# Optimization experiments

Hardware: AMD Instinct MI355X
Metric: run time of the kernel (lower is better)

Reference implementation:

```python
import jax, jax.numpy as jnp
import numpy as np

EMB = 512
HEAD = 8
HEAD_DIM = EMB // HEAD


def setup_inputs() -> dict:
    key = jax.random.key(0)
    ks = jax.random.split(key, 12)
    B, S = 2, 4096
    scale = 1.0 / np.sqrt(EMB)
    inp = {
        "q": jax.random.normal(ks[0], (B, S, EMB), dtype=jnp.float32),
        "kv": jax.random.normal(ks[1], (B, S, EMB), dtype=jnp.float32),
        "Wq": jax.random.normal(ks[2], (EMB, EMB), dtype=jnp.float32) * scale,
        "bq": jax.random.normal(ks[3], (EMB,), dtype=jnp.float32) * 0.01,
        "Wk": jax.random.normal(ks[4], (EMB, EMB), dtype=jnp.float32) * scale,
        "bk": jax.random.normal(ks[5], (EMB,), dtype=jnp.float32) * 0.01,
        "Wv": jax.random.normal(ks[6], (EMB, EMB), dtype=jnp.float32) * scale,
        "bv": jax.random.normal(ks[7], (EMB,), dtype=jnp.float32) * 0.01,
        "Wo": jax.random.normal(ks[8], (EMB, EMB), dtype=jnp.float32) * scale,
        "bo": jax.random.normal(ks[9], (EMB,), dtype=jnp.float32) * 0.01,
    }
    return inp


def reference(q, kv, Wq, bq, Wk, bk, Wv, bv, Wo, bo):
    B, N, _ = q.shape
    M = kv.shape[1]
    # Linear projections (torch Linear: x @ W^T + b)
    qh = (q @ Wq.T + bq).reshape(B, N, HEAD, HEAD_DIM).transpose(0, 2, 1, 3)  # [B,H,N,d]
    kh = (kv @ Wk.T + bk).reshape(B, M, HEAD, HEAD_DIM).transpose(0, 2, 1, 3)  # [B,H,M,d]
    vh = (kv @ Wv.T + bv).reshape(B, M, HEAD, HEAD_DIM).transpose(0, 2, 1, 3)  # [B,H,M,d]
    attn = jnp.einsum("bhnd,bhmd->bhnm", qh, kh) / jnp.sqrt(jnp.float32(HEAD_DIM))
    attn = jax.nn.softmax(attn, axis=-1)
    out = jnp.einsum("bhnm,bhmd->bhnd", attn, vh)  # [B,H,N,d]
    out = out.transpose(0, 2, 1, 3).reshape(B, N, EMB)
    out = out @ Wo.T + bo
    return out
```

## Files before the change

kernel.cpp:

```cpp
#include <hip/hip_runtime.h>
#include <stdint.h>

typedef unsigned short u16;
typedef __attribute__((ext_vector_type(8))) short short8;
typedef __attribute__((ext_vector_type(4))) float f32x4;
typedef __attribute__((ext_vector_type(16))) float f32x16;

typedef __attribute__((address_space(1))) void as1_void;
typedef __attribute__((address_space(3))) void as3_void;

__device__ inline u16 f2bf(float x) {
  uint32_t u = __float_as_uint(x);
  return (u16)((u + 0x7fffu + ((u >> 16) & 1u)) >> 16);
}

__device__ inline void gload16(const void* g, void* l) {
  __builtin_amdgcn_global_load_lds((as1_void*)g, (as3_void*)l, 16, 0, 0);
}

__device__ inline uint32_t cvtpk(float lo, float hi) {
  uint32_t d;
  asm("v_cvt_pk_bf16_f32 %0, %1, %2" : "=v"(d) : "v"(lo), "v"(hi));
  return d;
}

__device__ inline void plswap(uint32_t& a, uint32_t& b) {
  asm("v_permlane32_swap_b32 %0, %1" : "+v"(a), "+v"(b));
}

__device__ inline float fexp2(float x) {
  float r;
  asm("v_exp_f32 %0, %1" : "=v"(r) : "v"(x));
  return r;
}

__global__ __launch_bounds__(256) void cvt_all(const float* __restrict__ q,
                                               const float* __restrict__ kv,
                                               const float* __restrict__ Wq,
                                               const float* __restrict__ Wk,
                                               const float* __restrict__ Wv,
                                               const float* __restrict__ Wo,
                                               u16* __restrict__ qb,
                                               u16* __restrict__ kvb,
                                               u16* __restrict__ wall) {
  const int bx = blockIdx.x;
  const float* in;
  u16* out;
  int i;
  if (bx < 4096) {
    in = q; out = qb; i = bx * 256 + threadIdx.x;
  } else if (bx < 8192) {
    in = kv; out = kvb; i = (bx - 4096) * 256 + threadIdx.x;
  } else {
    int widx = (bx - 8192) >> 8;
    in = (widx == 0) ? Wq : (widx == 1) ? Wk : (widx == 2) ? Wv : Wo;
    out = wall + (size_t)widx * 262144;
    i = ((bx - 8192) & 255) * 256 + threadIdx.x;
  }
  float4 v = ((const float4*)in)[i];
  ushort4 o;
  o.x = f2bf(v.x); o.y = f2bf(v.y); o.z = f2bf(v.z); o.w = f2bf(v.w);
  ((ushort4*)out)[i] = o;
}

__global__ __launch_bounds__(256) void gemm_qkv(const u16* __restrict__ qb,
                                                const u16* __restrict__ kvb,
                                                const u16* __restrict__ wq,
                                                const u16* __restrict__ wk,
                                                const u16* __restrict__ wv,
                                                const float* __restrict__ bq,
                                                const float* __restrict__ bk,
                                                const float* __restrict__ bv,
                                                u16* __restrict__ Qh,
                                                u16* __restrict__ Kh,
                                                u16* __restrict__ Vt, float qscale) {
  __shared__ u16 Al[128 * 32];
  __shared__ u16 Wl[128 * 32];
  const int z = blockIdx.z;
  const u16* A = (z == 0) ? qb : kvb;
  const u16* W = (z == 0) ? wq : (z == 1) ? wk : wv;
  const float* bias = (z == 0) ? bq : (z == 1) ? bk : bv;
  const float prescale = (z == 0) ? qscale : 1.0f;
  u16* Cout = (z == 0) ? Qh : (z == 1) ? Kh : Vt;

  const int tid = threadIdx.x;
  const int lane = tid & 63;
  const int wv_ = tid >> 6;
  const int c = lane & 15;
  const int g = lane >> 4;
  const int wr = wv_ >> 1, wc = wv_ & 1;
  const int m0 = blockIdx.x * 128;
  const int n0 = blockIdx.y * 128;

  f32x4 acc[4][4];
#pragma unroll
  for (int i = 0; i < 4; i++)
#pragma unroll
    for (int j = 0; j < 4; j++) acc[i][j] = (f32x4){0.f, 0.f, 0.f, 0.f};

  for (int kk = 0; kk < 512; kk += 32) {
    __syncthreads();
    {
      int t0 = tid;
      int r0 = t0 >> 2, c0 = t0 & 3;
      gload16(A + (size_t)(m0 + r0) * 512 + kk + c0 * 8, (char*)Al + (size_t)(wv_ * 64) * 16);
      gload16(W + (size_t)(n0 + r0) * 512 + kk + c0 * 8, (char*)Wl + (size_t)(wv_ * 64) * 16);
      int t1 = 256 + tid;
      int r1 = t1 >> 2, c1 = t1 & 3;
      gload16(A + (size_t)(m0 + r1) * 512 + kk + c1 * 8, (char*)Al + (size_t)(256 + wv_ * 64) * 16);
      gload16(W + (size_t)(n0 + r1) * 512 + kk + c1 * 8, (char*)Wl + (size_t)(256 + wv_ * 64) * 16);
    }
    __syncthreads();

    short8 af[4], wf[4];
#pragma unroll
    for (int ai = 0; ai < 4; ai++)
      af[ai] = *(const short8*)&Al[(wr * 64 + ai * 16 + c) * 32 + g * 8];
#pragma unroll
    for (int bj = 0; bj < 4; bj++)
      wf[bj] = *(const short8*)&Wl[(wc * 64 + bj * 16 + c) * 32 + g * 8];
#pragma unroll
    for (int ai = 0; ai < 4; ai++)
#pragma unroll
      for (int bj = 0; bj < 4; bj++)
        acc[ai][bj] = __builtin_amdgcn_mfma_f32_16x16x32_bf16(af[ai], wf[bj], acc[ai][bj], 0, 0, 0);
  }

#pragma unroll
  for (int ai = 0; ai < 4; ai++)
#pragma unroll
    for (int bj = 0; bj < 4; bj++)
#pragma unroll
      for (int r = 0; r < 4; r++) {
        int m = m0 + wr * 64 + ai * 16 + g * 4 + r;
        int n = n0 + wc * 64 + bj * 16 + c;
        float v = (acc[ai][bj][r] + bias[n]) * prescale;
        int b = m >> 12, s = m & 4095;
        int h = n >> 6, d = n & 63;
        size_t idx;
        if (z < 2)
          idx = ((size_t)(b * 8 + h) * 4096 + s) * 64 + d;
        else
          idx = ((size_t)(b * 8 + h) * 64 + d) * 4096 + s;
        Cout[idx] = f2bf(v);
      }
}

__global__ __launch_bounds__(256) void gemm_out(const u16* __restrict__ A,
                                                const u16* __restrict__ W,
                                                const float* __restrict__ bias,
                                                float* __restrict__ Cout) {
  __shared__ u16 Al[128 * 32];
  __shared__ u16 Wl[128 * 32];
  const int tid = threadIdx.x;
  const int lane = tid & 63;
  const int wv_ = tid >> 6;
  const int c = lane & 15;
  const int g = lane >> 4;
  const int wr = wv_ >> 1, wc = wv_ & 1;
  const int m0 = blockIdx.x * 128;
  const int n0 = blockIdx.y * 128;

  f32x4 acc[4][4];
#pragma unroll
  for (int i = 0; i < 4; i++)
#pragma unroll
    for (int j = 0; j < 4; j++) acc[i][j] = (f32x4){0.f, 0.f, 0.f, 0.f};

  for (int kk = 0; kk < 512; kk += 32) {
    __syncthreads();
    {
      int t0 = tid;
      int r0 = t0 >> 2, c0 = t0 & 3;
      gload16(A + (size_t)(m0 + r0) * 512 + kk + c0 * 8, (char*)Al + (size_t)(wv_ * 64) * 16);
      gload16(W + (size_t)(n0 + r0) * 512 + kk + c0 * 8, (char*)Wl + (size_t)(wv_ * 64) * 16);
      int t1 = 256 + tid;
      int r1 = t1 >> 2, c1 = t1 & 3;
      gload16(A + (size_t)(m0 + r1) * 512 + kk + c1 * 8, (char*)Al + (size_t)(256 + wv_ * 64) * 16);
      gload16(W + (size_t)(n0 + r1) * 512 + kk + c1 * 8, (char*)Wl + (size_t)(256 + wv_ * 64) * 16);
    }
    __syncthreads();

    short8 af[4], wf[4];
#pragma unroll
    for (int ai = 0; ai < 4; ai++)
      af[ai] = *(const short8*)&Al[(wr * 64 + ai * 16 + c) * 32 + g * 8];
#pragma unroll
    for (int bj = 0; bj < 4; bj++)
      wf[bj] = *(const short8*)&Wl[(wc * 64 + bj * 16 + c) * 32 + g * 8];
#pragma unroll
    for (int ai = 0; ai < 4; ai++)
#pragma unroll
      for (int bj = 0; bj < 4; bj++)
        acc[ai][bj] = __builtin_amdgcn_mfma_f32_16x16x32_bf16(af[ai], wf[bj], acc[ai][bj], 0, 0, 0);
  }

#pragma unroll
  for (int ai = 0; ai < 4; ai++)
#pragma unroll
    for (int bj = 0; bj < 4; bj++)
#pragma unroll
      for (int r = 0; r < 4; r++) {
        int m = m0 + wr * 64 + ai * 16 + g * 4 + r;
        int n = n0 + wc * 64 + bj * 16 + c;
        Cout[(size_t)m * 512 + n] = acc[ai][bj][r] + bias[n];
      }
}

__global__ __launch_bounds__(256) void attn_split(const u16* __restrict__ Qh,
                                                  const u16* __restrict__ Kh,
                                                  const u16* __restrict__ Vt,
                                                  float* __restrict__ Op,
                                                  float* __restrict__ Ml) {
  __shared__ __align__(16) char smem[32768];
  const int tid = threadIdx.x;
  const int lane = tid & 63;
  const int w = tid >> 6;
  const int c5 = lane & 31;
  const int h = lane >> 5;
  const int bid = (blockIdx.x & 7) * 128 + (blockIdx.x >> 3);
  const int half = bid & 1;
  const int qt = (bid >> 1) & 31;
  const int bh = bid >> 6;
  const int q0 = qt * 128 + w * 32;
  const u16* Qb = Qh + (size_t)bh * 262144;
  const u16* Kb = Kh + (size_t)bh * 262144 + (size_t)half * 2048 * 64;
  const u16* Vb = Vt + (size_t)bh * 262144 + half * 2048;

  short8 qf[4];
#pragma unroll
  for (int kd = 0; kd < 4; kd++)
    qf[kd] = *(const short8*)(Qb + (size_t)(q0 + c5) * 64 + kd * 16 + h * 8);

  f32x16 accO[2];
#pragma unroll
  for (int i = 0; i < 16; i++) { accO[0][i] = 0.f; accO[1][i] = 0.f; }
  float l_r = 0.f;

  const int r = tid >> 4, p = tid & 15;
  const int x = p ^ r;
  const int gb = x >> 3, ge = x & 7;
  const u16* srcKA = Kb + (size_t)(r + 32 * gb) * 64 + ge * 8;
  const u16* srcKB = Kb + (size_t)(16 + r + 32 * gb) * 64 + ge * 8;
  const u16* srcVA = Vb + (size_t)(r + 32 * gb) * 4096 + ge * 8;
  const u16* srcVB = Vb + (size_t)(16 + r + 32 * gb) * 4096 + ge * 8;

#define ATTN_STAGE(BUF, T)                                \
  {                                                       \
    char* b_ = (char*)smem + (BUF)*16384 + w * 1024;      \
    gload16(srcKA + (size_t)(T)*4096, b_);                \
    gload16(srcKB + (size_t)(T)*4096, b_ + 4096);         \
    gload16(srcVA + (T)*64, b_ + 8192);                   \
    gload16(srcVB + (T)*64, b_ + 12288);                  \
  }

  ATTN_STAGE(0, 0)
  __syncthreads();
  int cur = 0;
  const int swz = c5 & 15;
  const int rowb = c5 * 128;

  for (int t = 0; t < 32; ++t) {
    if (t < 31) ATTN_STAGE(cur ^ 1, t + 1)

    const u16* Kl = (const u16*)(smem + cur * 16384);
    const u16* Vl = Kl + 4096;

    f32x16 s0, s1;
#pragma unroll
    for (int i = 0; i < 16; i++) { s0[i] = 0.f; s1[i] = 0.f; }
    __builtin_amdgcn_s_setprio(1);
#pragma unroll
    for (int kd = 0; kd < 4; kd++) {
      short8 kf0 = *(const short8*)&Kl[rowb + ((((kd << 1) + h) ^ swz) << 3)];
      short8 kf1 = *(const short8*)&Kl[rowb + (((8 + (kd << 1) + h) ^ swz) << 3)];
      s0 = __builtin_amdgcn_mfma_f32_32x32x16_bf16(kf0, qf[kd], s0, 0, 0, 0);
      s1 = __builtin_amdgcn_mfma_f32_32x32x16_bf16(kf1, qf[kd], s1, 0, 0, 0);
    }
    __builtin_amdgcn_s_setprio(0);

#pragma unroll
    for (int i = 0; i < 16; i++) { s0[i] = fexp2(s0[i]); s1[i] = fexp2(s1[i]); }

    float tsum0 = ((s0[0] + s1[0]) + (s0[4] + s1[4])) + ((s0[8] + s1[8]) + (s0[12] + s1[12]));
    float tsum1 = ((s0[1] + s1[1]) + (s0[5] + s1[5])) + ((s0[9] + s1[9]) + (s0[13] + s1[13]));
    float tsum2 = ((s0[2] + s1[2]) + (s0[6] + s1[6])) + ((s0[10] + s1[10]) + (s0[14] + s1[14]));
    float tsum3 = ((s0[3] + s1[3]) + (s0[7] + s1[7])) + ((s0[11] + s1[11]) + (s0[15] + s1[15]));
    float rsq = (tsum0 + tsum1) + (tsum2 + tsum3);
    l_r += rsq + __shfl_xor(rsq, 32);

    uint32_t pk0[4][2], pk1[4][2];
#pragma unroll
    for (int u = 0; u < 4; u++) {
      pk0[u][0] = cvtpk(s0[4 * u], s0[4 * u + 1]);
      pk0[u][1] = cvtpk(s0[4 * u + 2], s0[4 * u + 3]);
      pk1[u][0] = cvtpk(s1[4 * u], s1[4 * u + 1]);
      pk1[u][1] = cvtpk(s1[4 * u + 2], s1[4 * u + 3]);
    }
    short8 pa[4];
#pragma unroll
    for (int km = 0; km < 2; km++) {
      const int uA = (km & 1) * 2, uB = uA + 1;
      uint32_t a0 = pk0[uA][0], b0 = pk0[uB][0]; plswap(a0, b0);
      uint32_t a1 = pk0[uA][1], b1 = pk0[uB][1]; plswap(a1, b1);
      union { uint32_t u[4]; short8 s; } uu;
      uu.u[0] = a0; uu.u[1] = a1; uu.u[2] = b0; uu.u[3] = b1;
      pa[km] = uu.s;
    }
#pragma unroll
    for (int km = 2; km < 4; km++) {
      const int uA = (km & 1) * 2, uB = uA + 1;
      uint32_t a0 = pk1[uA][0], b0 = pk1[uB][0]; plswap(a0, b0);
      uint32_t a1 = pk1[uA][1], b1 = pk1[uB][1]; plswap(a1, b1);
      union { uint32_t u[4]; short8 s; } uu;
      uu.u[0] = a0; uu.u[1] = a1; uu.u[2] = b0; uu.u[3] = b1;
      pa[km] = uu.s;
    }

    __builtin_amdgcn_s_setprio(1);
#pragma unroll
    for (int km = 0; km < 4; km++) {
      short8 vf0 = *(const short8*)&Vl[rowb + ((((km << 1) + h) ^ swz) << 3)];
      short8 vf1 = *(const short8*)&Vl[rowb + (((8 + (km << 1) + h) ^ swz) << 3)];
      accO[0] = __builtin_amdgcn_mfma_f32_32x32x16_bf16(vf0, pa[km], accO[0], 0, 0, 0);
      accO[1] = __builtin_amdgcn_mfma_f32_32x32x16_bf16(vf1, pa[km], accO[1], 0, 0, 0);
    }
    __builtin_amdgcn_s_setprio(0);

    __syncthreads();
    cur ^= 1;
  }

  const size_t pbase = (size_t)(half * 16 + bh) * 4096 + q0 + c5;
  float* Opw = Op + pbase * 64;
#pragma unroll
  for (int db = 0; db < 2; db++)
#pragma unroll
    for (int rr = 0; rr < 16; rr++) {
      int d = db * 32 + 4 * h + (rr & 3) + 8 * (rr >> 2);
      Opw[d] = accO[db][rr];
    }
  if (h == 0) { Ml[pbase * 2] = 0.f; Ml[pbase * 2 + 1] = l_r; }
}

__global__ __launch_bounds__(256) void attn_combine(const float* __restrict__ Op,
                                                    const float* __restrict__ Ml,
                                                    u16* __restrict__ aO) {
  int tg = blockIdx.x * 256 + threadIdx.x;
  int bhq = tg >> 3, seg = tg & 7;
  const float* p0 = Op + (size_t)bhq * 64 + seg * 8;
  const float* p1 = p0 + 4194304;
  float m0 = Ml[bhq * 2], l0 = Ml[bhq * 2 + 1];
  float m1 = Ml[131072 + bhq * 2], l1 = Ml[131072 + bhq * 2 + 1];
  float ms = fmaxf(m0, m1);
  float a0 = fexp2(m0 - ms), a1 = fexp2(m1 - ms);
  float inv = 1.f / (l0 * a0 + l1 * a1);
  float4 x0 = ((const float4*)p0)[0], x1 = ((const float4*)p0)[1];
  float4 y0 = ((const float4*)p1)[0], y1 = ((const float4*)p1)[1];
  ushort4 o0, o1;
  o0.x = f2bf((x0.x * a0 + y0.x * a1) * inv);
  o0.y = f2bf((x0.y * a0 + y0.y * a1) * inv);
  o0.z = f2bf((x0.z * a0 + y0.z * a1) * inv);
  o0.w = f2bf((x0.w * a0 + y0.w * a1) * inv);
  o1.x = f2bf((x1.x * a0 + y1.x * a1) * inv);
  o1.y = f2bf((x1.y * a0 + y1.y * a1) * inv);
  o1.z = f2bf((x1.z * a0 + y1.z * a1) * inv);
  o1.w = f2bf((x1.w * a0 + y1.w * a1) * inv);
  int bh = bhq >> 12, q = bhq & 4095;
  int b = bh >> 3, hh = bh & 7;
  u16* dst = aO + ((size_t)(b * 4096 + q)) * 512 + hh * 64 + seg * 8;
  ((ushort4*)dst)[0] = o0;
  ((ushort4*)dst)[1] = o1;
}

extern "C" void kernel_launch(void* const* d_in, const int* in_sizes, int n_in,
                              void* d_out, int out_size, void* d_ws, size_t ws_size,
                              hipStream_t stream) {
  const float* q  = (const float*)d_in[0];
  const float* kv = (const float*)d_in[1];
  const float* Wq = (const float*)d_in[2];
  const float* bq = (const float*)d_in[3];
  const float* Wk = (const float*)d_in[4];
  const float* bk = (const float*)d_in[5];
  const float* Wv = (const float*)d_in[6];
  const float* bv = (const float*)d_in[7];
  const float* Wo = (const float*)d_in[8];
  const float* bo = (const float*)d_in[9];

  const size_t MB = 1u << 20;
  char* ws = (char*)d_ws;
  u16* qb  = (u16*)(ws + 0 * MB);
  u16* kvb = (u16*)(ws + 8 * MB);
  u16* wqb = (u16*)(ws + 16 * MB);
  u16* wkb = (u16*)(ws + 16 * MB + 524288);
  u16* wvb = (u16*)(ws + 17 * MB);
  u16* wob = (u16*)(ws + 17 * MB + 524288);
  u16* Qh  = (u16*)(ws + 18 * MB);
  u16* Kh  = (u16*)(ws + 26 * MB);
  u16* Vt  = (u16*)(ws + 34 * MB);
  u16* aO  = (u16*)(ws + 42 * MB);
  float* Op = (float*)(ws + 50 * MB);
  float* Ml = (float*)(ws + 84 * MB);

  cvt_all<<<dim3(9216), dim3(256), 0, stream>>>(q, kv, Wq, Wk, Wv, Wo, qb, kvb, wqb);

  const float qscale = 0.125f * 1.44269504088896340736f;
  gemm_qkv<<<dim3(64, 4, 3), dim3(256), 0, stream>>>(qb, kvb, wqb, wkb, wvb,
                                                     bq, bk, bv, Qh, Kh, Vt, qscale);

  attn_split<<<dim3(1024), dim3(256), 0, stream>>>(Qh, Kh, Vt, Op, Ml);
  attn_combine<<<dim3(2048), dim3(256), 0, stream>>>(Op, Ml, aO);

  gemm_out<<<dim3(64, 4), dim3(256), 0, stream>>>(aO, wob, bo, (float*)d_out);
}
```

Measured before the change: 151.3 us.

## Software-pipeline PV MFMAs one tile behind QK to overlap softmax

Restructures the attention loop so the P·V MFMAs for tile t-1 run right after the QK MFMAs of tile t, before the exp/convert work. V fragments and packed probabilities are held in registers across iterations, and an epilogue finishes the last tile. The aim is to overlap the exp and pack VALU work with MFMA execution and to hide LDS read latency. In exchange it raises register pressure (8 short8 V fragments plus 4 P fragments live across the barrier), which may reduce occupancy.

```diff
diff --git a/kernel.cpp b/kernel.cpp
--- a/kernel.cpp
+++ b/kernel.cpp
@@ -256,11 +256,14 @@
 
   ATTN_STAGE(0, 0)
   __syncthreads();
-  int cur = 0;
   const int swz = c5 & 15;
   const int rowb = c5 * 128;
 
+  short8 pa_prev[4];
+  short8 vf_prev[8];
+
   for (int t = 0; t < 32; ++t) {
+    const int cur = t & 1;
     if (t < 31) ATTN_STAGE(cur ^ 1, t + 1)
 
     const u16* Kl = (const u16*)(smem + cur * 16384);
@@ -277,7 +280,15 @@
       s0 = __builtin_amdgcn_mfma_f32_32x32x16_bf16(kf0, qf[kd], s0, 0, 0, 0);
       s1 = __builtin_amdgcn_mfma_f32_32x32x16_bf16(kf1, qf[kd], s1, 0, 0, 0);
     }
+    if (t > 0) {
+#pragma unroll
+      for (int km = 0; km < 4; km++) {
+        accO[0] = __builtin_amdgcn_mfma_f32_32x32x16_bf16(vf_prev[2 * km], pa_prev[km], accO[0], 0, 0, 0);
+        accO[1] = __builtin_amdgcn_mfma_f32_32x32x16_bf16(vf_prev[2 * km + 1], pa_prev[km], accO[1], 0, 0, 0);
+      }
+    }
     __builtin_amdgcn_s_setprio(0);
+    __builtin_amdgcn_sched_barrier(0);
 
 #pragma unroll
     for (int i = 0; i < 16; i++) { s0[i] = fexp2(s0[i]); s1[i] = fexp2(s1[i]); }
@@ -297,7 +308,6 @@
       pk1[u][0] = cvtpk(s1[4 * u], s1[4 * u + 1]);
       pk1[u][1] = cvtpk(s1[4 * u + 2], s1[4 * u + 3]);
     }
-    short8 pa[4];
 #pragma unroll
     for (int km = 0; km < 2; km++) {
       const int uA = (km & 1) * 2, uB = uA + 1;
@@ -305,7 +315,7 @@
       uint32_t a1 = pk0[uA][1], b1 = pk0[uB][1]; plswap(a1, b1);
       union { uint32_t u[4]; short8 s; } uu;
       uu.u[0] = a0; uu.u[1] = a1; uu.u[2] = b0; uu.u[3] = b1;
-      pa[km] = uu.s;
+      pa_prev[km] = uu.s;
     }
 #pragma unroll
     for (int km = 2; km < 4; km++) {
@@ -314,21 +324,22 @@
       uint32_t a1 = pk1[uA][1], b1 = pk1[uB][1]; plswap(a1, b1);
       union { uint32_t u[4]; short8 s; } uu;
       uu.u[0] = a0; uu.u[1] = a1; uu.u[2] = b0; uu.u[3] = b1;
-      pa[km] = uu.s;
-    }
-
-    __builtin_amdgcn_s_setprio(1);
+      pa_prev[km] = uu.s;
+    }
+
 #pragma unroll
     for (int km = 0; km < 4; km++) {
-      short8 vf0 = *(const short8*)&Vl[rowb + ((((km << 1) + h) ^ swz) << 3)];
-      short8 vf1 = *(const short8*)&Vl[rowb + (((8 + (km << 1) + h) ^ swz) << 3)];
-      accO[0] = __builtin_amdgcn_mfma_f32_32x32x16_bf16(vf0, pa[km], accO[0], 0, 0, 0);
-      accO[1] = __builtin_amdgcn_mfma_f32_32x32x16_bf16(vf1, pa[km], accO[1], 0, 0, 0);
-    }
-    __builtin_amdgcn_s_setprio(0);
+      vf_prev[2 * km]     = *(const short8*)&Vl[rowb + ((((km << 1) + h) ^ swz) << 3)];
+      vf_prev[2 * km + 1] = *(const short8*)&Vl[rowb + (((8 + (km << 1) + h) ^ swz) << 3)];
+    }
 
     __syncthreads();
-    cur ^= 1;
+  }
+
+#pragma unroll
+  for (int km = 0; km < 4; km++) {
+    accO[0] = __builtin_amdgcn_mfma_f32_32x32x16_bf16(vf_prev[2 * km], pa_prev[km], accO[0], 0, 0, 0);
+    accO[1] = __builtin_amdgcn_mfma_f32_32x32x16_bf16(vf_prev[2 * km + 1], pa_prev[km], accO[1], 0, 0, 0);
   }
 
   const size_t pbase = (size_t)(half * 16 + bh) * 4096 + q0 + c5;
```

Result: faster. 142.6 us (-5.7%).
